# Kernel tuning notes

Hardware: AMD Instinct MI355X
Metric: run time of the kernel (lower is better)

## Reference

```python
import jax, jax.numpy as jnp
import numpy as np

N_NODES = 50000
N_EDGES = 500000
NEG_SLOPE = 0.2


def gat_layer(x, src, dst, W, a_src, a_dst, b, n):
    """PyG-style GATConv (add_self_loops=True, concat=True, eval mode).
    x: [N, F_in], W: [F_in, H*C], a_src/a_dst: [H, C], b: [H*C]."""
    H, C = a_src.shape
    h = (x @ W).reshape(-1, H, C)              # [N, H, C]
    loops = jnp.arange(n, dtype=src.dtype)
    s = jnp.concatenate([src, loops])          # self-loops appended
    d = jnp.concatenate([dst, loops])
    alpha_src = jnp.einsum('nhc,hc->nh', h, a_src)   # [N, H]
    alpha_dst = jnp.einsum('nhc,hc->nh', h, a_dst)
    e = jax.nn.leaky_relu(alpha_src[s] + alpha_dst[d], NEG_SLOPE)  # [E+N, H]
    m = jax.ops.segment_max(e, d, num_segments=n)    # segment softmax over dst
    w = jnp.exp(e - m[d])
    denom = jax.ops.segment_sum(w, d, num_segments=n)
    attn = w / (denom[d] + 1e-16)                    # [E+N, H]
    msg = h[s] * attn[:, :, None]                    # [E+N, H, C]
    out = jax.ops.segment_sum(msg, d, num_segments=n)  # [N, H, C]
    return out.reshape(n, H * C) + b


def setup_inputs() -> dict:
    key = jax.random.key(0)
    ks = jax.random.split(key, 20)
    F_in, Hd, Hh = 128, 64, 4
    g = lambda k, shp, fan: jax.random.normal(k, shp, jnp.float32) * (1.0 / np.sqrt(fan))
    inp = {
        'x': jax.random.normal(ks[0], (N_NODES, F_in), jnp.float32),
        'edge_index': jax.random.randint(ks[1], (2, N_EDGES), 0, N_NODES, jnp.int32),
        'W1': g(ks[2], (F_in, Hh * Hd), F_in),
        'a1s': g(ks[3], (Hh, Hd), Hd), 'a1d': g(ks[4], (Hh, Hd), Hd),
        'b1': jnp.zeros((Hh * Hd,), jnp.float32),
        'W2': g(ks[5], (Hh * Hd, Hh * Hd), Hh * Hd),
        'a2s': g(ks[6], (Hh, Hd), Hd), 'a2d': g(ks[7], (Hh, Hd), Hd),
        'b2': jnp.zeros((Hh * Hd,), jnp.float32),
        'W3': g(ks[8], (Hh * Hd, Hd), Hh * Hd),
        'a3s': g(ks[9], (1, Hd), Hd), 'a3d': g(ks[10], (1, Hd), Hd),
        'b3': jnp.zeros((Hd,), jnp.float32),
        'cW1': g(ks[11], (Hd, Hd // 2), Hd), 'cb1': jnp.zeros((Hd // 2,), jnp.float32),
        'cW2': g(ks[12], (Hd // 2, 2), Hd // 2), 'cb2': jnp.zeros((2,), jnp.float32),
    }
    return inp


def reference(x, edge_index, W1, a1s, a1d, b1, W2, a2s, a2d, b2,
              W3, a3s, a3d, b3, cW1, cb1, cW2, cb2):
    n = x.shape[0]
    src, dst = edge_index[0], edge_index[1]
    h = jax.nn.elu(gat_layer(x, src, dst, W1, a1s, a1d, b1, n))
    h = jax.nn.elu(gat_layer(h, src, dst, W2, a2s, a2d, b2, n))
    h = jax.nn.relu(gat_layer(h, src, dst, W3, a3s, a3d, b3, n))
    h = jax.nn.relu(h @ cW1 + cb1)
    logits = h @ cW2 + cb2
    return jax.nn.log_softmax(logits, axis=1)
```

## Files before the change

kernel.cpp:

```cpp
#include <hip/hip_runtime.h>
#include <hip/hip_fp16.h>

#define LRELU(v) ((v) > 0.f ? (v) : 0.2f * (v))

typedef _Float16 f16x8 __attribute__((ext_vector_type(8)));
typedef float f32x4 __attribute__((ext_vector_type(4)));

__device__ __forceinline__ f16x8 f16x8_zero() {
    f16x8 v;
#pragma unroll
    for (int j = 0; j < 8; ++j) v[j] = (_Float16)0.f;
    return v;
}

__global__ __launch_bounds__(256) void hist_kernel(const int* __restrict__ dst,
                                                   int* __restrict__ cnt, int E) {
    int e = blockIdx.x * 256 + threadIdx.x;
    if (e < E) atomicAdd(&cnt[dst[e]], 1);
}

__global__ __launch_bounds__(256) void scan_blk(const int* __restrict__ cnt,
                                                int* __restrict__ offv,
                                                int* __restrict__ bsum, int N) {
    __shared__ int sh[256];
    const int t = threadIdx.x;
    const int base = blockIdx.x * 1024 + t * 4;
    int v0 = (base + 0 < N) ? cnt[base + 0] : 0;
    int v1 = (base + 1 < N) ? cnt[base + 1] : 0;
    int v2 = (base + 2 < N) ? cnt[base + 2] : 0;
    int v3 = (base + 3 < N) ? cnt[base + 3] : 0;
    const int T = v0 + v1 + v2 + v3;
    sh[t] = T;
    __syncthreads();
    for (int o = 1; o < 256; o <<= 1) {
        int x = (t >= o) ? sh[t - o] : 0;
        __syncthreads();
        sh[t] += x;
        __syncthreads();
    }
    const int excl = sh[t] - T;
    if (t == 255) bsum[blockIdx.x] = sh[255];
    if (base + 0 < N) offv[base + 0] = excl;
    if (base + 1 < N) offv[base + 1] = excl + v0;
    if (base + 2 < N) offv[base + 2] = excl + v0 + v1;
    if (base + 3 < N) offv[base + 3] = excl + v0 + v1 + v2;
}

__global__ __launch_bounds__(64) void scan_top(int* __restrict__ bsum,
                                               int* __restrict__ offv,
                                               int NB, int N) {
    const int t = threadIdx.x;
    const int v = (t < NB) ? bsum[t] : 0;
    int incl = v;
#pragma unroll
    for (int o = 1; o < 64; o <<= 1) {
        int x = __shfl_up(incl, o);
        if (t >= o) incl += x;
    }
    if (t < NB) bsum[t] = incl - v;
    if (t == NB - 1) offv[N] = incl;
}

__global__ __launch_bounds__(256) void scan_add(int* __restrict__ offv,
                                                const int* __restrict__ bsum, int N) {
    const int base = blockIdx.x * 1024 + threadIdx.x * 4;
    const int add = bsum[blockIdx.x];
#pragma unroll
    for (int i = 0; i < 4; ++i)
        if (base + i < N) offv[base + i] += add;
}

__global__ __launch_bounds__(256) void fill_kernel(const int* __restrict__ dst,
                                                   const int* __restrict__ srcv,
                                                   const int* __restrict__ offv,
                                                   int* __restrict__ cur,
                                                   int* __restrict__ csrsrc, int E) {
    int e = blockIdx.x * 256 + threadIdx.x;
    if (e < E) {
        int d = dst[e];
        int p = atomicAdd(&cur[d], 1);
        csrsrc[offv[d] + p] = srcv[e];
    }
}

__global__ __launch_bounds__(256) void prep_w16(const float* __restrict__ W,
                                                _Float16* __restrict__ wt,
                                                int K, int Nn) {
    int idx = blockIdx.x * 256 + threadIdx.x;
    if (idx < K * Nn) {
        int k = idx / Nn, nn2 = idx - k * Nn;
        wt[(size_t)nn2 * K + k] = (_Float16)W[idx];
    }
}

__global__ __launch_bounds__(256) void cvt_f16(const float* __restrict__ in,
                                               _Float16* __restrict__ out, int n4) {
    int i = blockIdx.x * 256 + threadIdx.x;
    if (i < n4) {
        float4 v = *(const float4*)(in + (size_t)i * 4);
        _Float16 o[4] = {(_Float16)v.x, (_Float16)v.y, (_Float16)v.z, (_Float16)v.w};
        *(float2*)(out + (size_t)i * 4) = *(float2*)o;
    }
}

template <int WM, int WN, int K, int H>
__global__ __launch_bounds__(WM * WN * 64) void gemm_f16_fused(
    const _Float16* __restrict__ A, const _Float16* __restrict__ Wt,
    const float* __restrict__ a_s, const float* __restrict__ a_d,
    _Float16* __restrict__ hout, float* __restrict__ als,
    float* __restrict__ ald, int M, int Nn) {
    constexpr int BM = WM * 64;
    constexpr int T = WM * WN * 64;
    constexpr int CHUNKS = BM * 16;
    __shared__ f16x8 Atile[BM * 16];
    const int t = threadIdx.x;
    const int lane = t & 63;
    const int wv = t >> 6;
    const int wm = wv / WN, wn = wv % WN;
    const int m0 = blockIdx.x * BM;
    const int n0 = blockIdx.y * (WN * 64);
    const int l15 = lane & 15, lg = lane >> 4;

    f32x4 acc[4][4];
    const f32x4 zz = {0.f, 0.f, 0.f, 0.f};
#pragma unroll
    for (int mi = 0; mi < 4; ++mi)
#pragma unroll
        for (int ni = 0; ni < 4; ++ni) acc[mi][ni] = zz;

    for (int kc = 0; kc < K; kc += 128) {
        __syncthreads();
#pragma unroll
        for (int i = 0; i < CHUNKS / T; ++i) {
            const int c = i * T + t;
            const int row = c >> 4, cc = c & 15;
            const int gr = m0 + row;
            f16x8 v = (gr < M) ? *(const f16x8*)(A + (size_t)gr * K + kc + cc * 8)
                               : f16x8_zero();
            Atile[(row * 16 + cc) ^ (row & 7)] = v;
        }
        __syncthreads();
#pragma unroll
        for (int ks = 0; ks < 4; ++ks) {
            f16x8 af[4], bf[4];
#pragma unroll
            for (int mi = 0; mi < 4; ++mi) {
                const int row = wm * 64 + mi * 16 + l15;
                af[mi] = Atile[(row * 16 + ks * 4 + lg) ^ (row & 7)];
            }
#pragma unroll
            for (int ni = 0; ni < 4; ++ni) {
                const int col = n0 + wn * 64 + ni * 16 + l15;
                bf[ni] = *(const f16x8*)(Wt + (size_t)col * K + kc + ks * 32 + lg * 8);
            }
#pragma unroll
            for (int mi = 0; mi < 4; ++mi)
#pragma unroll
                for (int ni = 0; ni < 4; ++ni)
                    acc[mi][ni] = __builtin_amdgcn_mfma_f32_16x16x32_f16(
                        af[mi], bf[ni], acc[mi][ni], 0, 0, 0);
        }
    }
    const int head = (n0 + wn * 64) >> 6;
    float a4s[4], a4d[4];
#pragma unroll
    for (int ni = 0; ni < 4; ++ni) {
        a4s[ni] = a_s[head * 64 + ni * 16 + l15];
        a4d[ni] = a_d[head * 64 + ni * 16 + l15];
    }
#pragma unroll
    for (int mi = 0; mi < 4; ++mi)
#pragma unroll
        for (int j = 0; j < 4; ++j) {
            const int r = m0 + wm * 64 + mi * 16 + lg * 4 + j;
            if (r < M) {
                float s1 = 0.f, s2 = 0.f;
#pragma unroll
                for (int ni = 0; ni < 4; ++ni) {
                    const float v = acc[mi][ni][j];
                    s1 += v * a4s[ni];
                    s2 += v * a4d[ni];
                    hout[(size_t)r * Nn + n0 + wn * 64 + ni * 16 + l15] = (_Float16)v;
                }
#pragma unroll
                for (int o = 8; o; o >>= 1) {
                    s1 += __shfl_xor(s1, o);
                    s2 += __shfl_xor(s2, o);
                }
                if (l15 == 0) {
                    als[(size_t)r * H + head] = s1;
                    ald[(size_t)r * H + head] = s2;
                }
            }
        }
}


__global__ __launch_bounds__(256) void gat_agg_h4(
    const __half* __restrict__ hhf, const float4* __restrict__ als4,
    const float4* __restrict__ ald4, const int* __restrict__ csrsrc,
    const int* __restrict__ offv, const float* __restrict__ bias,
    __half* __restrict__ outh, int N) {
    __shared__ int sidAll[4][64];
    __shared__ float wAll[4][64 * 4];
    const int wv = threadIdx.x >> 6;
    const int t = threadIdx.x & 63;
    const int n = blockIdx.x * 4 + wv;
    if (n >= N) return;
    const int hh = t >> 4;
    int* sid = sidAll[wv];
    float* wsh = wAll[wv];
    const int start = offv[n];
    const int deg = offv[n + 1] - start;
    const float4 ad = ald4[n];
    const float4 asf = als4[n];
    float wself;
    {
        float4 w4;
        w4.x = __expf(LRELU(asf.x + ad.x));
        w4.y = __expf(LRELU(asf.y + ad.y));
        w4.z = __expf(LRELU(asf.z + ad.z));
        w4.w = __expf(LRELU(asf.w + ad.w));
        float r = w4.x;
        r = (hh == 1) ? w4.y : r;
        r = (hh == 2) ? w4.z : r;
        r = (hh == 3) ? w4.w : r;
        wself = r;
    }
    float accA[4], accB[4] = {0.f, 0.f, 0.f, 0.f};
    {
        float2 raw = *(const float2*)(hhf + (size_t)n * 256 + t * 4);
        __half2 h0 = *(__half2*)&raw.x;
        __half2 h1 = *(__half2*)&raw.y;
        float2 a0 = __half22float2(h0), a1 = __half22float2(h1);
        accA[0] = a0.x * wself; accA[1] = a0.y * wself;
        accA[2] = a1.x * wself; accA[3] = a1.y * wself;
    }
    float dsA = wself, dsB = 0.f;

    for (int base = 0; base < deg; base += 64) {
        const int nb = min(64, deg - base);
        int s = 0;
        float4 w4 = {0.f, 0.f, 0.f, 0.f};
        if (t < nb) {
            s = csrsrc[start + base + t];
            const float4 av = als4[s];
            w4.x = __expf(LRELU(av.x + ad.x));
            w4.y = __expf(LRELU(av.y + ad.y));
            w4.z = __expf(LRELU(av.z + ad.z));
            w4.w = __expf(LRELU(av.w + ad.w));
        }
        sid[t] = s;
        *(float4*)(wsh + t * 4) = w4;
        __threadfence_block();
        int i = 0;
        for (; i + 1 < nb; i += 2) {
            const int sA = sid[i];
            const float wA = wsh[i * 4 + hh];
            const int sB = sid[i + 1];
            const float wB = wsh[(i + 1) * 4 + hh];
            float2 rA = *(const float2*)(hhf + (size_t)sA * 256 + t * 4);
            float2 rB = *(const float2*)(hhf + (size_t)sB * 256 + t * 4);
            __half2 a0 = *(__half2*)&rA.x, a1 = *(__half2*)&rA.y;
            __half2 b0 = *(__half2*)&rB.x, b1 = *(__half2*)&rB.y;
            float2 fa0 = __half22float2(a0), fa1 = __half22float2(a1);
            float2 fb0 = __half22float2(b0), fb1 = __half22float2(b1);
            dsA += wA; dsB += wB;
            accA[0] += fa0.x * wA; accA[1] += fa0.y * wA;
            accA[2] += fa1.x * wA; accA[3] += fa1.y * wA;
            accB[0] += fb0.x * wB; accB[1] += fb0.y * wB;
            accB[2] += fb1.x * wB; accB[3] += fb1.y * wB;
        }
        if (i < nb) {
            const int sA = sid[i];
            const float wA = wsh[i * 4 + hh];
            float2 rA = *(const float2*)(hhf + (size_t)sA * 256 + t * 4);
            __half2 a0 = *(__half2*)&rA.x, a1 = *(__half2*)&rA.y;
            float2 fa0 = __half22float2(a0), fa1 = __half22float2(a1);
            dsA += wA;
            accA[0] += fa0.x * wA; accA[1] += fa0.y * wA;
            accA[2] += fa1.x * wA; accA[3] += fa1.y * wA;
        }
        __threadfence_block();
    }
    const float inv = 1.f / (dsA + dsB + 1e-16f);
    const float4 bv = *(const float4*)(bias + t * 4);
    float4 o4;
    o4.x = (accA[0] + accB[0]) * inv + bv.x;
    o4.y = (accA[1] + accB[1]) * inv + bv.y;
    o4.z = (accA[2] + accB[2]) * inv + bv.z;
    o4.w = (accA[3] + accB[3]) * inv + bv.w;
    o4.x = (o4.x > 0.f) ? o4.x : (__expf(o4.x) - 1.f);
    o4.y = (o4.y > 0.f) ? o4.y : (__expf(o4.y) - 1.f);
    o4.z = (o4.z > 0.f) ? o4.z : (__expf(o4.z) - 1.f);
    o4.w = (o4.w > 0.f) ? o4.w : (__expf(o4.w) - 1.f);
    __half2 p0 = __floats2half2_rn(o4.x, o4.y);
    __half2 p1 = __floats2half2_rn(o4.z, o4.w);
    float2 st;
    *(__half2*)&st.x = p0;
    *(__half2*)&st.y = p1;
    *(float2*)(outh + (size_t)n * 256 + t * 4) = st;
}

__global__ __launch_bounds__(256) void gat_agg_h1_cls(
    const __half* __restrict__ hhf, const float* __restrict__ als,
    const float* __restrict__ ald, const int* __restrict__ csrsrc,
    const int* __restrict__ offv, const float* __restrict__ bias,
    const float* __restrict__ cW1, const float* __restrict__ cb1,
    const float* __restrict__ cW2, const float* __restrict__ cb2,
    float* __restrict__ outp, int N) {
    __shared__ float w1s[2048];
    __shared__ float w2s[64];
    __shared__ int sidAll[4][64];
    __shared__ float wAll[4][64];
    __shared__ float xsAll[4][64];
    for (int i = threadIdx.x; i < 2048; i += 256) w1s[i] = cW1[i];
    if (threadIdx.x < 64) w2s[threadIdx.x] = cW2[threadIdx.x];
    __syncthreads();
    const int wv = threadIdx.x >> 6;
    const int t = threadIdx.x & 63;
    const int n = blockIdx.x * 4 + wv;
    if (n >= N) return;
    int* sid = sidAll[wv];
    float* wsh = wAll[wv];
    float* xs = xsAll[wv];
    const int start = offv[n];
    const int deg = offv[n + 1] - start;
    const float ad = ald[n];
    const float wself = __expf(LRELU(als[n] + ad));
    float accA = __half2float(hhf[(size_t)n * 64 + t]) * wself;
    float accB = 0.f;
    float dsA = wself, dsB = 0.f;

    for (int base = 0; base < deg; base += 64) {
        const int nb = min(64, deg - base);
        int s = 0;
        float w = 0.f;
        if (t < nb) {
            s = csrsrc[start + base + t];
            w = __expf(LRELU(als[s] + ad));
        }
        sid[t] = s;
        wsh[t] = w;
        __threadfence_block();
        int i = 0;
        for (; i + 1 < nb; i += 2) {
            const int sA = sid[i];
            const float wA = wsh[i];
            const int sB = sid[i + 1];
            const float wB = wsh[i + 1];
            const float hA = __half2float(hhf[(size_t)sA * 64 + t]);
            const float hB = __half2float(hhf[(size_t)sB * 64 + t]);
            dsA += wA; dsB += wB;
            accA += hA * wA;
            accB += hB * wB;
        }
        if (i < nb) {
            const int sA = sid[i];
            const float wA = wsh[i];
            dsA += wA;
            accA += __half2float(hhf[(size_t)sA * 64 + t]) * wA;
        }
        __threadfence_block();
    }
    const float val = fmaxf((accA + accB) / (dsA + dsB + 1e-16f) + bias[t], 0.f);
    xs[t] = val;
    __threadfence_block();
    const int j = t & 31;
    const int half = t >> 5;
    float s1 = 0.f;
#pragma unroll
    for (int cc = 0; cc < 32; ++cc) {
        const int c = half * 32 + cc;
        s1 += xs[c] * w1s[c * 32 + j];
    }
    s1 += __shfl_xor(s1, 32);
    const float hid = fmaxf(s1 + cb1[j], 0.f);
    const int k = t & 1, jj = t >> 1;
    const float hjj = __shfl(hid, jj);
    float s2 = hjj * w2s[jj * 2 + k];
#pragma unroll
    for (int o = 2; o < 64; o <<= 1) s2 += __shfl_xor(s2, o);
    s2 += cb2[k];
    const float a = __shfl(s2, 0);
    const float b = __shfl(s2, 1);
    const float mm = fmaxf(a, b);
    const float lse = mm + logf(__expf(a - mm) + __expf(b - mm));
    if (t < 2) outp[(size_t)n * 2 + t] = s2 - lse;
}

extern "C" void kernel_launch(void* const* d_in, const int* in_sizes, int n_in,
                              void* d_out, int out_size, void* d_ws, size_t ws_size,
                              hipStream_t stream) {
    const float* x   = (const float*)d_in[0];
    const int*   ei  = (const int*)d_in[1];
    const float* W1  = (const float*)d_in[2];
    const float* a1s = (const float*)d_in[3];
    const float* a1d = (const float*)d_in[4];
    const float* b1  = (const float*)d_in[5];
    const float* W2  = (const float*)d_in[6];
    const float* a2s = (const float*)d_in[7];
    const float* a2d = (const float*)d_in[8];
    const float* b2  = (const float*)d_in[9];
    const float* W3  = (const float*)d_in[10];
    const float* a3s = (const float*)d_in[11];
    const float* a3d = (const float*)d_in[12];
    const float* b3  = (const float*)d_in[13];
    const float* cW1 = (const float*)d_in[14];
    const float* cb1 = (const float*)d_in[15];
    const float* cW2 = (const float*)d_in[16];
    const float* cb2 = (const float*)d_in[17];

    const int N = in_sizes[0] / 128;
    const int E = in_sizes[1] / 2;
    const int* srcv = ei;
    const int* dstv = ei + E;

    char* p = (char*)d_ws;
    _Float16* slotA = (_Float16*)p; p += (size_t)N * 256 * 2;
    _Float16* slotB = (_Float16*)p; p += (size_t)N * 256 * 2;
    _Float16* slotC = (_Float16*)p; p += (size_t)N * 128 * 2;
    float* als = (float*)p; p += (size_t)N * 4 * 4;
    float* ald = (float*)p; p += (size_t)N * 4 * 4;
    int* cnt = (int*)p; p += (size_t)N * 4;
    int* offv = (int*)p; p += (size_t)(N + 4) * 4;
    int* csr = (int*)p; p += (size_t)E * 4;
    _Float16* Wt1 = (_Float16*)p; p += (size_t)128 * 256 * 2;
    _Float16* Wt2 = (_Float16*)p; p += (size_t)256 * 256 * 2;
    _Float16* Wt3 = (_Float16*)p; p += (size_t)256 * 64 * 2;
    int* bsum = (int*)p;

    prep_w16<<<(128 * 256 + 255) / 256, 256, 0, stream>>>(W1, Wt1, 128, 256);
    prep_w16<<<(256 * 256 + 255) / 256, 256, 0, stream>>>(W2, Wt2, 256, 256);
    prep_w16<<<(256 * 64 + 255) / 256, 256, 0, stream>>>(W3, Wt3, 256, 64);
    cvt_f16<<<(N * 128 / 4 + 255) / 256, 256, 0, stream>>>(x, slotC, N * 128 / 4);

    const int NB = (N + 1023) / 1024;
    hipMemsetAsync(cnt, 0, (size_t)N * sizeof(int), stream);
    hist_kernel<<<(E + 255) / 256, 256, 0, stream>>>(dstv, cnt, E);
    scan_blk<<<NB, 256, 0, stream>>>(cnt, offv, bsum, N);
    scan_top<<<1, 64, 0, stream>>>(bsum, offv, NB, N);
    scan_add<<<NB, 256, 0, stream>>>(offv, bsum, N);
    hipMemsetAsync(cnt, 0, (size_t)N * sizeof(int), stream);
    fill_kernel<<<(E + 255) / 256, 256, 0, stream>>>(dstv, srcv, offv, cnt, csr, E);

    const int MB128 = (N + 127) / 128;
    const int MB256 = (N + 255) / 256;
    const int AGG = (N + 3) / 4;

    gemm_f16_fused<2, 4, 128, 4><<<dim3(MB128, 1), 512, 0, stream>>>(
        slotC, Wt1, a1s, a1d, slotA, als, ald, N, 256);
    gat_agg_h4<<<AGG, 256, 0, stream>>>((const __half*)slotA, (const float4*)als,
                                        (const float4*)ald, csr, offv, b1,
                                        (__half*)slotB, N);

    gemm_f16_fused<2, 4, 256, 4><<<dim3(MB128, 1), 512, 0, stream>>>(
        slotB, Wt2, a2s, a2d, slotA, als, ald, N, 256);
    gat_agg_h4<<<AGG, 256, 0, stream>>>((const __half*)slotA, (const float4*)als,
                                        (const float4*)ald, csr, offv, b2,
                                        (__half*)slotB, N);

    gemm_f16_fused<4, 1, 256, 1><<<dim3(MB256, 1), 256, 0, stream>>>(
        slotB, Wt3, a3s, a3d, slotA, als, ald, N, 64);
    gat_agg_h1_cls<<<AGG, 256, 0, stream>>>((const __half*)slotA, als, ald, csr,
                                            offv, b3, cW1, cb1, cW2, cb2,
                                            (float*)d_out, N);
}
```

Before: 288.9 us.

## Fuse input conversion into GEMM, merge weight prep, unroll aggregation gathers by four

The separate fp32-to-fp16 conversion pass over x is removed; the first GEMM now loads fp32 rows and converts them while filling shared memory. The three weight-transpose launches become one kernel. Attention logits are prescaled by log2(e) so the aggregation kernels can use the hardware exp2. The aggregation loops gather four neighbours per iteration using transposed shared weights and vector loads, and the softmax denominator becomes a per-lane partial sum reduced once at the end instead of a per-edge accumulation. These changes cut launches and memory traffic, at the cost of more registers in the unrolled loops.

```diff
diff --git a/kernel.cpp b/kernel.cpp
--- a/kernel.cpp
+++ b/kernel.cpp
@@ -2,9 +2,15 @@
 #include <hip/hip_fp16.h>
 
 #define LRELU(v) ((v) > 0.f ? (v) : 0.2f * (v))
+#define LOG2E 1.44269504088896340736f
 
 typedef _Float16 f16x8 __attribute__((ext_vector_type(8)));
+typedef _Float16 f16x4 __attribute__((ext_vector_type(4)));
 typedef float f32x4 __attribute__((ext_vector_type(4)));
+
+__device__ __forceinline__ float fexp2(float x) {
+    return __builtin_amdgcn_exp2f(x);
+}
 
 __device__ __forceinline__ f16x8 f16x8_zero() {
     f16x8 v;
@@ -83,29 +89,29 @@
     }
 }
 
-__global__ __launch_bounds__(256) void prep_w16(const float* __restrict__ W,
-                                                _Float16* __restrict__ wt,
-                                                int K, int Nn) {
+__global__ __launch_bounds__(256) void prep_w_all(
+    const float* __restrict__ W1, const float* __restrict__ W2,
+    const float* __restrict__ W3, _Float16* __restrict__ Wt1,
+    _Float16* __restrict__ Wt2, _Float16* __restrict__ Wt3) {
+    const int S1 = 128 * 256, S2 = 256 * 256, S3 = 256 * 64;
     int idx = blockIdx.x * 256 + threadIdx.x;
-    if (idx < K * Nn) {
-        int k = idx / Nn, nn2 = idx - k * Nn;
-        wt[(size_t)nn2 * K + k] = (_Float16)W[idx];
-    }
-}
-
-__global__ __launch_bounds__(256) void cvt_f16(const float* __restrict__ in,
-                                               _Float16* __restrict__ out, int n4) {
-    int i = blockIdx.x * 256 + threadIdx.x;
-    if (i < n4) {
-        float4 v = *(const float4*)(in + (size_t)i * 4);
-        _Float16 o[4] = {(_Float16)v.x, (_Float16)v.y, (_Float16)v.z, (_Float16)v.w};
-        *(float2*)(out + (size_t)i * 4) = *(float2*)o;
-    }
-}
-
-template <int WM, int WN, int K, int H>
+    if (idx < S1) {
+        int k = idx >> 8, nn = idx & 255;
+        Wt1[nn * 128 + k] = (_Float16)W1[idx];
+    } else if (idx < S1 + S2) {
+        int i = idx - S1;
+        int k = i >> 8, nn = i & 255;
+        Wt2[nn * 256 + k] = (_Float16)W2[idx - S1];
+    } else if (idx < S1 + S2 + S3) {
+        int i = idx - S1 - S2;
+        int k = i >> 6, nn = i & 63;
+        Wt3[nn * 256 + k] = (_Float16)W3[i];
+    }
+}
+
+template <int WM, int WN, int K, int H, bool AF32>
 __global__ __launch_bounds__(WM * WN * 64) void gemm_f16_fused(
-    const _Float16* __restrict__ A, const _Float16* __restrict__ Wt,
+    const void* __restrict__ Av, const _Float16* __restrict__ Wt,
     const float* __restrict__ a_s, const float* __restrict__ a_d,
     _Float16* __restrict__ hout, float* __restrict__ als,
     float* __restrict__ ald, int M, int Nn) {
@@ -113,6 +119,8 @@
     constexpr int T = WM * WN * 64;
     constexpr int CHUNKS = BM * 16;
     __shared__ f16x8 Atile[BM * 16];
+    const _Float16* A16 = (const _Float16*)Av;
+    const float* A32 = (const float*)Av;
     const int t = threadIdx.x;
     const int lane = t & 63;
     const int wv = t >> 6;
@@ -135,8 +143,21 @@
             const int c = i * T + t;
             const int row = c >> 4, cc = c & 15;
             const int gr = m0 + row;
-            f16x8 v = (gr < M) ? *(const f16x8*)(A + (size_t)gr * K + kc + cc * 8)
-                               : f16x8_zero();
+            f16x8 v;
+            if (gr < M) {
+                if constexpr (AF32) {
+                    float4 p = *(const float4*)(A32 + (size_t)gr * K + kc + cc * 8);
+                    float4 q = *(const float4*)(A32 + (size_t)gr * K + kc + cc * 8 + 4);
+                    v[0] = (_Float16)p.x; v[1] = (_Float16)p.y;
+                    v[2] = (_Float16)p.z; v[3] = (_Float16)p.w;
+                    v[4] = (_Float16)q.x; v[5] = (_Float16)q.y;
+                    v[6] = (_Float16)q.z; v[7] = (_Float16)q.w;
+                } else {
+                    v = *(const f16x8*)(A16 + (size_t)gr * K + kc + cc * 8);
+                }
+            } else {
+                v = f16x8_zero();
+            }
             Atile[(row * 16 + cc) ^ (row & 7)] = v;
         }
         __syncthreads();
@@ -165,8 +186,8 @@
     float a4s[4], a4d[4];
 #pragma unroll
     for (int ni = 0; ni < 4; ++ni) {
-        a4s[ni] = a_s[head * 64 + ni * 16 + l15];
-        a4d[ni] = a_d[head * 64 + ni * 16 + l15];
+        a4s[ni] = a_s[head * 64 + ni * 16 + l15] * LOG2E;
+        a4d[ni] = a_d[head * 64 + ni * 16 + l15] * LOG2E;
     }
 #pragma unroll
     for (int mi = 0; mi < 4; ++mi)
@@ -196,47 +217,46 @@
 }
 
 
+__device__ __forceinline__ float sel4(float4 v, int h) {
+    float r = v.x;
+    r = (h == 1) ? v.y : r;
+    r = (h == 2) ? v.z : r;
+    r = (h == 3) ? v.w : r;
+    return r;
+}
+
 __global__ __launch_bounds__(256) void gat_agg_h4(
-    const __half* __restrict__ hhf, const float4* __restrict__ als4,
+    const _Float16* __restrict__ hhf, const float4* __restrict__ als4,
     const float4* __restrict__ ald4, const int* __restrict__ csrsrc,
     const int* __restrict__ offv, const float* __restrict__ bias,
-    __half* __restrict__ outh, int N) {
+    _Float16* __restrict__ outh, int N) {
     __shared__ int sidAll[4][64];
-    __shared__ float wAll[4][64 * 4];
+    __shared__ float wTAll[4][4][64];
     const int wv = threadIdx.x >> 6;
     const int t = threadIdx.x & 63;
     const int n = blockIdx.x * 4 + wv;
     if (n >= N) return;
     const int hh = t >> 4;
     int* sid = sidAll[wv];
-    float* wsh = wAll[wv];
+    float (*wT)[64] = wTAll[wv];
     const int start = offv[n];
     const int deg = offv[n + 1] - start;
     const float4 ad = ald4[n];
     const float4 asf = als4[n];
-    float wself;
+    float4 ws4;
+    ws4.x = fexp2(LRELU(asf.x + ad.x));
+    ws4.y = fexp2(LRELU(asf.y + ad.y));
+    ws4.z = fexp2(LRELU(asf.z + ad.z));
+    ws4.w = fexp2(LRELU(asf.w + ad.w));
+    const float wself = sel4(ws4, hh);
+    float accA[4], accB[4] = {};
     {
-        float4 w4;
-        w4.x = __expf(LRELU(asf.x + ad.x));
-        w4.y = __expf(LRELU(asf.y + ad.y));
-        w4.z = __expf(LRELU(asf.z + ad.z));
-        w4.w = __expf(LRELU(asf.w + ad.w));
-        float r = w4.x;
-        r = (hh == 1) ? w4.y : r;
-        r = (hh == 2) ? w4.z : r;
-        r = (hh == 3) ? w4.w : r;
-        wself = r;
-    }
-    float accA[4], accB[4] = {0.f, 0.f, 0.f, 0.f};
-    {
-        float2 raw = *(const float2*)(hhf + (size_t)n * 256 + t * 4);
-        __half2 h0 = *(__half2*)&raw.x;
-        __half2 h1 = *(__half2*)&raw.y;
-        float2 a0 = __half22float2(h0), a1 = __half22float2(h1);
-        accA[0] = a0.x * wself; accA[1] = a0.y * wself;
-        accA[2] = a1.x * wself; accA[3] = a1.y * wself;
-    }
-    float dsA = wself, dsB = 0.f;
+        const f16x4 hv = *(const f16x4*)(hhf + (size_t)n * 256 + t * 4);
+#pragma unroll
+        for (int c = 0; c < 4; ++c) accA[c] = (float)hv[c] * wself;
+    }
+    float4 wacc = {0.f, 0.f, 0.f, 0.f};
+    if (t == 0) wacc = ws4;
 
     for (int base = 0; base < deg; base += 64) {
         const int nb = min(64, deg - base);
@@ -245,65 +265,68 @@
         if (t < nb) {
             s = csrsrc[start + base + t];
             const float4 av = als4[s];
-            w4.x = __expf(LRELU(av.x + ad.x));
-            w4.y = __expf(LRELU(av.y + ad.y));
-            w4.z = __expf(LRELU(av.z + ad.z));
-            w4.w = __expf(LRELU(av.w + ad.w));
+            w4.x = fexp2(LRELU(av.x + ad.x));
+            w4.y = fexp2(LRELU(av.y + ad.y));
+            w4.z = fexp2(LRELU(av.z + ad.z));
+            w4.w = fexp2(LRELU(av.w + ad.w));
+            wacc.x += w4.x; wacc.y += w4.y;
+            wacc.z += w4.z; wacc.w += w4.w;
         }
         sid[t] = s;
-        *(float4*)(wsh + t * 4) = w4;
+        wT[0][t] = w4.x;
+        wT[1][t] = w4.y;
+        wT[2][t] = w4.z;
+        wT[3][t] = w4.w;
         __threadfence_block();
         int i = 0;
-        for (; i + 1 < nb; i += 2) {
-            const int sA = sid[i];
-            const float wA = wsh[i * 4 + hh];
-            const int sB = sid[i + 1];
-            const float wB = wsh[(i + 1) * 4 + hh];
-            float2 rA = *(const float2*)(hhf + (size_t)sA * 256 + t * 4);
-            float2 rB = *(const float2*)(hhf + (size_t)sB * 256 + t * 4);
-            __half2 a0 = *(__half2*)&rA.x, a1 = *(__half2*)&rA.y;
-            __half2 b0 = *(__half2*)&rB.x, b1 = *(__half2*)&rB.y;
-            float2 fa0 = __half22float2(a0), fa1 = __half22float2(a1);
-            float2 fb0 = __half22float2(b0), fb1 = __half22float2(b1);
-            dsA += wA; dsB += wB;
-            accA[0] += fa0.x * wA; accA[1] += fa0.y * wA;
-            accA[2] += fa1.x * wA; accA[3] += fa1.y * wA;
-            accB[0] += fb0.x * wB; accB[1] += fb0.y * wB;
-            accB[2] += fb1.x * wB; accB[3] += fb1.y * wB;
-        }
-        if (i < nb) {
-            const int sA = sid[i];
-            const float wA = wsh[i * 4 + hh];
-            float2 rA = *(const float2*)(hhf + (size_t)sA * 256 + t * 4);
-            __half2 a0 = *(__half2*)&rA.x, a1 = *(__half2*)&rA.y;
-            float2 fa0 = __half22float2(a0), fa1 = __half22float2(a1);
-            dsA += wA;
-            accA[0] += fa0.x * wA; accA[1] += fa0.y * wA;
-            accA[2] += fa1.x * wA; accA[3] += fa1.y * wA;
+        for (; i + 3 < nb; i += 4) {
+            const int4 ss = *(const int4*)&sid[i];
+            const float4 ww = *(const float4*)&wT[hh][i];
+            const f16x4 h0 = *(const f16x4*)(hhf + (size_t)ss.x * 256 + t * 4);
+            const f16x4 h1 = *(const f16x4*)(hhf + (size_t)ss.y * 256 + t * 4);
+            const f16x4 h2 = *(const f16x4*)(hhf + (size_t)ss.z * 256 + t * 4);
+            const f16x4 h3 = *(const f16x4*)(hhf + (size_t)ss.w * 256 + t * 4);
+#pragma unroll
+            for (int c = 0; c < 4; ++c) {
+                accA[c] += (float)h0[c] * ww.x;
+                accB[c] += (float)h1[c] * ww.y;
+                accA[c] += (float)h2[c] * ww.z;
+                accB[c] += (float)h3[c] * ww.w;
+            }
+        }
+        for (; i < nb; ++i) {
+            const int s0 = sid[i];
+            const float w0 = wT[hh][i];
+            const f16x4 h0 = *(const f16x4*)(hhf + (size_t)s0 * 256 + t * 4);
+#pragma unroll
+            for (int c = 0; c < 4; ++c) accA[c] += (float)h0[c] * w0;
         }
         __threadfence_block();
     }
-    const float inv = 1.f / (dsA + dsB + 1e-16f);
+#pragma unroll
+    for (int o = 32; o; o >>= 1) {
+        wacc.x += __shfl_xor(wacc.x, o);
+        wacc.y += __shfl_xor(wacc.y, o);
+        wacc.z += __shfl_xor(wacc.z, o);
+        wacc.w += __shfl_xor(wacc.w, o);
+    }
+    const float inv = 1.f / (sel4(wacc, hh) + 1e-16f);
     const float4 bv = *(const float4*)(bias + t * 4);
-    float4 o4;
-    o4.x = (accA[0] + accB[0]) * inv + bv.x;
-    o4.y = (accA[1] + accB[1]) * inv + bv.y;
-    o4.z = (accA[2] + accB[2]) * inv + bv.z;
-    o4.w = (accA[3] + accB[3]) * inv + bv.w;
-    o4.x = (o4.x > 0.f) ? o4.x : (__expf(o4.x) - 1.f);
-    o4.y = (o4.y > 0.f) ? o4.y : (__expf(o4.y) - 1.f);
-    o4.z = (o4.z > 0.f) ? o4.z : (__expf(o4.z) - 1.f);
-    o4.w = (o4.w > 0.f) ? o4.w : (__expf(o4.w) - 1.f);
-    __half2 p0 = __floats2half2_rn(o4.x, o4.y);
-    __half2 p1 = __floats2half2_rn(o4.z, o4.w);
-    float2 st;
-    *(__half2*)&st.x = p0;
-    *(__half2*)&st.y = p1;
-    *(float2*)(outh + (size_t)n * 256 + t * 4) = st;
+    float o4[4];
+#pragma unroll
+    for (int c = 0; c < 4; ++c) o4[c] = (accA[c] + accB[c]) * inv;
+    o4[0] += bv.x; o4[1] += bv.y; o4[2] += bv.z; o4[3] += bv.w;
+#pragma unroll
+    for (int c = 0; c < 4; ++c)
+        o4[c] = (o4[c] > 0.f) ? o4[c] : (__expf(o4[c]) - 1.f);
+    f16x4 st;
+#pragma unroll
+    for (int c = 0; c < 4; ++c) st[c] = (_Float16)o4[c];
+    *(f16x4*)(outh + (size_t)n * 256 + t * 4) = st;
 }
 
 __global__ __launch_bounds__(256) void gat_agg_h1_cls(
-    const __half* __restrict__ hhf, const float* __restrict__ als,
+    const _Float16* __restrict__ hhf, const float* __restrict__ als,
     const float* __restrict__ ald, const int* __restrict__ csrsrc,
     const int* __restrict__ offv, const float* __restrict__ bias,
     const float* __restrict__ cW1, const float* __restrict__ cb1,
@@ -327,10 +350,10 @@
     const int start = offv[n];
     const int deg = offv[n + 1] - start;
     const float ad = ald[n];
-    const float wself = __expf(LRELU(als[n] + ad));
-    float accA = __half2float(hhf[(size_t)n * 64 + t]) * wself;
-    float accB = 0.f;
-    float dsA = wself, dsB = 0.f;
+    const float wself = fexp2(LRELU(als[n] + ad));
+    float a0 = (float)hhf[(size_t)n * 64 + t] * wself;
+    float a1 = 0.f, a2 = 0.f, a3 = 0.f;
+    float wacc = (t == 0) ? wself : 0.f;
 
     for (int base = 0; base < deg; base += 64) {
         const int nb = min(64, deg - base);
@@ -338,32 +361,29 @@
         float w = 0.f;
         if (t < nb) {
             s = csrsrc[start + base + t];
-            w = __expf(LRELU(als[s] + ad));
+            w = fexp2(LRELU(als[s] + ad));
+            wacc += w;
         }
         sid[t] = s;
         wsh[t] = w;
         __threadfence_block();
         int i = 0;
-        for (; i + 1 < nb; i += 2) {
-            const int sA = sid[i];
-            const float wA = wsh[i];
-            const int sB = sid[i + 1];
-            const float wB = wsh[i + 1];
-            const float hA = __half2float(hhf[(size_t)sA * 64 + t]);
-            const float hB = __half2float(hhf[(size_t)sB * 64 + t]);
-            dsA += wA; dsB += wB;
-            accA += hA * wA;
-            accB += hB * wB;
-        }
-        if (i < nb) {
-            const int sA = sid[i];
-            const float wA = wsh[i];
-            dsA += wA;
-            accA += __half2float(hhf[(size_t)sA * 64 + t]) * wA;
+        for (; i + 3 < nb; i += 4) {
+            const int4 ss = *(const int4*)&sid[i];
+            const float4 ww = *(const float4*)&wsh[i];
+            a0 += (float)hhf[(size_t)ss.x * 64 + t] * ww.x;
+            a1 += (float)hhf[(size_t)ss.y * 64 + t] * ww.y;
+            a2 += (float)hhf[(size_t)ss.z * 64 + t] * ww.z;
+            a3 += (float)hhf[(size_t)ss.w * 64 + t] * ww.w;
+        }
+        for (; i < nb; ++i) {
+            a0 += (float)hhf[(size_t)sid[i] * 64 + t] * wsh[i];
         }
         __threadfence_block();
     }
-    const float val = fmaxf((accA + accB) / (dsA + dsB + 1e-16f) + bias[t], 0.f);
+#pragma unroll
+    for (int o = 32; o; o >>= 1) wacc += __shfl_xor(wacc, o);
+    const float val = fmaxf((a0 + a1 + a2 + a3) / (wacc + 1e-16f) + bias[t], 0.f);
     xs[t] = val;
     __threadfence_block();
     const int j = t & 31;
@@ -419,7 +439,6 @@
     char* p = (char*)d_ws;
     _Float16* slotA = (_Float16*)p; p += (size_t)N * 256 * 2;
     _Float16* slotB = (_Float16*)p; p += (size_t)N * 256 * 2;
-    _Float16* slotC = (_Float16*)p; p += (size_t)N * 128 * 2;
     float* als = (float*)p; p += (size_t)N * 4 * 4;
     float* ald = (float*)p; p += (size_t)N * 4 * 4;
     int* cnt = (int*)p; p += (size_t)N * 4;
@@ -430,10 +449,8 @@
     _Float16* Wt3 = (_Float16*)p; p += (size_t)256 * 64 * 2;
     int* bsum = (int*)p;
 
-    prep_w16<<<(128 * 256 + 255) / 256, 256, 0, stream>>>(W1, Wt1, 128, 256);
-    prep_w16<<<(256 * 256 + 255) / 256, 256, 0, stream>>>(W2, Wt2, 256, 256);
-    prep_w16<<<(256 * 64 + 255) / 256, 256, 0, stream>>>(W3, Wt3, 256, 64);
-    cvt_f16<<<(N * 128 / 4 + 255) / 256, 256, 0, stream>>>(x, slotC, N * 128 / 4);
+    prep_w_all<<<(128 * 256 + 256 * 256 + 256 * 64 + 255) / 256, 256, 0, stream>>>(
+        W1, W2, W3, Wt1, Wt2, Wt3);
 
     const int NB = (N + 1023) / 1024;
     hipMemsetAsync(cnt, 0, (size_t)N * sizeof(int), stream);
@@ -448,21 +465,21 @@
     const int MB256 = (N + 255) / 256;
     const int AGG = (N + 3) / 4;
 
-    gemm_f16_fused<2, 4, 128, 4><<<dim3(MB128, 1), 512, 0, stream>>>(
-        slotC, Wt1, a1s, a1d, slotA, als, ald, N, 256);
-    gat_agg_h4<<<AGG, 256, 0, stream>>>((const __half*)slotA, (const float4*)als,
+    gemm_f16_fused<2, 4, 128, 4, true><<<dim3(MB128, 1), 512, 0, stream>>>(
+        x, Wt1, a1s, a1d, slotA, als, ald, N, 256);
+    gat_agg_h4<<<AGG, 256, 0, stream>>>(slotA, (const float4*)als,
                                         (const float4*)ald, csr, offv, b1,
-                                        (__half*)slotB, N);
-
-    gemm_f16_fused<2, 4, 256, 4><<<dim3(MB128, 1), 512, 0, stream>>>(
+                                        slotB, N);
+
+    gemm_f16_fused<2, 4, 256, 4, false><<<dim3(MB128, 1), 512, 0, stream>>>(
         slotB, Wt2, a2s, a2d, slotA, als, ald, N, 256);
-    gat_agg_h4<<<AGG, 256, 0, stream>>>((const __half*)slotA, (const float4*)als,
+    gat_agg_h4<<<AGG, 256, 0, stream>>>(slotA, (const float4*)als,
                                         (const float4*)ald, csr, offv, b2,
-                                        (__half*)slotB, N);
-
-    gemm_f16_fused<4, 1, 256, 1><<<dim3(MB256, 1), 256, 0, stream>>>(
+                                        slotB, N);
+
+    gemm_f16_fused<4, 1, 256, 1, false><<<dim3(MB256, 1), 256, 0, stream>>>(
         slotB, Wt3, a3s, a3d, slotA, als, ald, N, 64);
-    gat_agg_h1_cls<<<AGG, 256, 0, stream>>>((const __half*)slotA, als, ald, csr,
+    gat_agg_h1_cls<<<AGG, 256, 0, stream>>>(slotA, als, ald, csr,
                                             offv, b3, cW1, cb1, cW2, cb2,
                                             (float*)d_out, N);
 }
```

New measurement: 275.0 us. 4.8% less time.
